# Performance work log

Hardware: AMD Instinct MI355X
Metric: run time of the kernel (lower is better)

The kernel has to match this reference:

```python
import jax, jax.numpy as jnp
import numpy as np

D_FEATURE = 512
D_K = 512
B, LQ, N = 64, 128, 2048
NEG_BIAS = 1e10


def setup_inputs() -> dict:
    key = jax.random.key(0)
    k1, k2, k3, k4, k5, k6 = jax.random.split(key, 6)
    # xavier_uniform bound for Linear(d_feature -> d_k), weight shape [d_k, d_feature]
    bound = float(np.sqrt(6.0 / (D_FEATURE + D_K)))
    metal_feature = jax.random.normal(k1, (B, LQ, D_FEATURE), dtype=jnp.float32)
    x = jax.random.normal(k2, (B, N, D_FEATURE), dtype=jnp.float32)
    mask = jax.random.randint(k3, (B, N), 0, 2, dtype=jnp.int32)
    W_q = jax.random.uniform(k4, (D_K, D_FEATURE), jnp.float32, -bound, bound)
    W_k = jax.random.uniform(k5, (D_K, D_FEATURE), jnp.float32, -bound, bound)
    W_v = jax.random.uniform(k6, (D_K, D_FEATURE), jnp.float32, -bound, bound)
    return {"metal_feature": metal_feature, "x": x, "mask": mask,
            "W_q": W_q, "W_k": W_k, "W_v": W_v}


def reference(metal_feature, x, mask, W_q, W_k, W_v):
    # Q: [B, Lq, d_k], K/V: [B, N, d_k]  (torch Linear: y = x @ W.T, no bias)
    Q = jnp.einsum('blf,kf->blk', metal_feature, W_q)
    K = jnp.einsum('bnf,kf->bnk', x, W_k)
    V = jnp.einsum('bnf,kf->bnk', x, W_v)
    scale = 1.0 / jnp.sqrt(jnp.float32(D_K))
    # scores: [B, Lq, N] with additive mask bias (mask broadcast over queries)
    scores = jnp.einsum('blk,bnk->bln', Q, K) * scale
    scores = scores - (1.0 - mask[:, None, :].astype(scores.dtype)) * NEG_BIAS
    attn = jax.nn.softmax(scores, axis=-1)
    out = jnp.einsum('bln,bnk->blk', attn, V)
    # relu; squeeze(1) is a no-op for Lq>1; dropout identity at eval
    return jax.nn.relu(out)
```

## Files before the change

### kernel.cpp

```cpp
#include <hip/hip_runtime.h>

typedef __attribute__((ext_vector_type(4))) float   f32x4;
typedef __attribute__((ext_vector_type(8))) __bf16  bf16x8;
typedef unsigned short u16;
typedef __attribute__((ext_vector_type(8))) unsigned short u16x8;
typedef __attribute__((ext_vector_type(4))) unsigned short u16x4;

__device__ __forceinline__ u16 f2bf(float f) {
  unsigned u = __builtin_bit_cast(unsigned, f);
  u += 0x7fffu + ((u >> 16) & 1u);
  return (u16)(u >> 16);
}
__device__ __forceinline__ float bf2f(u16 h) {
  unsigned u = ((unsigned)h) << 16;
  return __builtin_bit_cast(float, u);
}
__device__ __forceinline__ void gld16(const void* g, void* l) {
  __builtin_amdgcn_global_load_lds(
      (const __attribute__((address_space(1))) void*)g,
      (__attribute__((address_space(3))) void*)l, 16, 0, 0);
}


#define SB __builtin_amdgcn_sched_barrier(0)
#define SYNC_MID do { SB; __builtin_amdgcn_s_barrier(); \
  asm volatile("s_waitcnt lgkmcnt(0)" ::: "memory"); SB; } while(0)
#define SYNC_END do { SB; __builtin_amdgcn_s_barrier(); SB; } while(0)
#define VM4 do { SB; asm volatile("s_waitcnt vmcnt(4)" ::: "memory"); SB; } while(0)
#define VM0 do { SB; asm volatile("s_waitcnt vmcnt(0)" ::: "memory"); SB; } while(0)

#define LDA(AQ, S, I0) \
  _Pragma("unroll") for (int f = 0; f < 2; ++f) \
  _Pragma("unroll") for (int s = 0; s < 2; ++s) { \
    const int rl = ((I0)+f)*16 + lr; \
    AQ[f*2+s] = *(const u16x8*)&SM[((S)*2 + wr)*8192 + rl*64 + (((s*4+lc) ^ (rl&7))*8)]; }

#define LDB(S) \
  _Pragma("unroll") for (int j = 0; j < 4; ++j) \
  _Pragma("unroll") for (int s = 0; s < 2; ++s) { \
    const int rl = (wc&1)*64 + j*16 + lr; \
    bq[j][s] = *(const u16x8*)&SM[32768 + ((S)*2 + (wc>>1))*8192 + rl*64 + (((s*4+lc) ^ (rl&7))*8)]; }

#define MM(AQ, I0) do { \
  _Pragma("unroll") for (int f = 0; f < 2; ++f) \
  _Pragma("unroll") for (int j = 0; j < 4; ++j) \
  _Pragma("unroll") for (int s = 0; s < 2; ++s) \
    acc[(I0)+f][j] = __builtin_amdgcn_mfma_f32_16x16x32_bf16( \
      __builtin_bit_cast(bf16x8, AQ[f*2+s]), __builtin_bit_cast(bf16x8, bq[j][s]), \
      acc[(I0)+f][j], 0, 0, 0); \
  } while(0)

__global__ __launch_bounds__(512, 1)
void kv8_k(const u16* __restrict__ xb, const u16* __restrict__ Wkv,
           u16* __restrict__ Kc, u16* __restrict__ Vt)
{
  __shared__ u16 SM[65536];
  const int t = threadIdx.x;
  const int w = t >> 6, lane = t & 63;
  const int wr = w >> 2, wc = w & 3;
  const int lr = lane & 15, lc = lane >> 4;

  int bx, by;
  if (gridDim.y == 64) {
    const int h = (int)(blockIdx.y * 4 + blockIdx.x);
    const int c = h & 7, i = h >> 3;
    by = c + 8 * (i & 7);
    bx = i >> 3;
  } else { bx = blockIdx.x; by = blockIdx.y; }
  const int n0 = bx * 256;
  const u16* xg = xb + (long)by * 2048 * 512;

  f32x4 acc[8][4];
#pragma unroll
  for (int i = 0; i < 8; i++)
#pragma unroll
    for (int j = 0; j < 4; j++) acc[i][j] = f32x4{0.f, 0.f, 0.f, 0.f};
  u16x8 bq[4][2];

  auto stageA = [&](int TT, int h) {
#pragma unroll
    for (int r = 0; r < 2; ++r) {
      const int c = r * 512 + t;
      const int row = c >> 3, slot = c & 7;
      const u16* g = xg + (long)((TT >> 3) * 256 + h * 128 + row) * 512
                        + (TT & 7) * 64 + ((slot ^ (row & 7)) * 8);
      gld16(g, (void*)&SM[((TT & 1) * 2 + h) * 8192 + c * 8]);
    }
  };
  auto stageB = [&](int TT, int h) {
#pragma unroll
    for (int r = 0; r < 2; ++r) {
      const int c = r * 512 + t;
      const int row = c >> 3, slot = c & 7;
      const u16* g = Wkv + (long)(n0 + h * 128 + row) * 512
                         + (TT & 7) * 64 + ((slot ^ (row & 7)) * 8);
      gld16(g, (void*)&SM[32768 + ((TT & 1) * 2 + h) * 8192 + c * 8]);
    }
  };
  auto epi = [&](int mt) {
#pragma unroll
    for (int i = 0; i < 8; i++)
#pragma unroll
      for (int j = 0; j < 4; j++) {
        const int ml = mt * 256 + wr * 128 + i * 16 + lc * 4;
        const int n  = n0 + wc * 64 + j * 16 + lr;
        if (n0 < 512) {
#pragma unroll
          for (int ii = 0; ii < 4; ii++)
            Kc[((long)by * 2048 + ml + ii) * 512 + n] = f2bf(acc[i][j][ii]);
        } else {
          u16x4 hh;
#pragma unroll
          for (int ii = 0; ii < 4; ii++) hh[ii] = f2bf(acc[i][j][ii]);
          *(u16x4*)(Vt + ((long)by * 512 + (n - 512)) * 2048 + ml) = hh;
        }
        acc[i][j] = f32x4{0.f, 0.f, 0.f, 0.f};
      }
  };

  stageA(0, 0); stageA(0, 1);
  stageB(0, 0); stageB(0, 1);
  stageB(1, 0); stageB(1, 1);
  VM4;
  __builtin_amdgcn_s_barrier(); SB;

  const int NT = 64;
#pragma unroll 1
  for (int I = 0; I < NT / 2; ++I) {
    const int a = 2 * I, b = 2 * I + 1;
    const bool g2 = (a + 2) < NT;
    const bool g3 = (b + 2) < NT;
    { u16x8 aqX[4], aqY[4];
      LDB(0); LDA(aqX, 0, 0); LDA(aqY, 0, 2);
      stageA(b, 0); stageA(b, 1);
      SYNC_MID;
      __builtin_amdgcn_s_setprio(1); MM(aqX, 0); MM(aqY, 2); __builtin_amdgcn_s_setprio(0);
      SYNC_END; }
    { u16x8 aqX[4], aqY[4];
      LDA(aqX, 0, 4); LDA(aqY, 0, 6);
      if (g2) { stageB(a + 2, 0); stageB(a + 2, 1); }
      SYNC_MID;
      __builtin_amdgcn_s_setprio(1); MM(aqX, 4); MM(aqY, 6); __builtin_amdgcn_s_setprio(0);
      if (g2) { VM4; } else { VM0; }
      SYNC_END; }
    { u16x8 aqX[4], aqY[4];
      LDB(1); LDA(aqX, 1, 0); LDA(aqY, 1, 2);
      if (g2) { stageA(a + 2, 0); stageA(a + 2, 1); }
      SYNC_MID;
      __builtin_amdgcn_s_setprio(1); MM(aqX, 0); MM(aqY, 2); __builtin_amdgcn_s_setprio(0);
      SYNC_END; }
    { u16x8 aqX[4], aqY[4];
      LDA(aqX, 1, 4); LDA(aqY, 1, 6);
      if (g3) { stageB(b + 2, 0); stageB(b + 2, 1); }
      SYNC_MID;
      __builtin_amdgcn_s_setprio(1); MM(aqX, 4); MM(aqY, 6); __builtin_amdgcn_s_setprio(0);
      if (g3) { VM4; } else { VM0; }
      SYNC_END; }
    if ((I & 3) == 3) epi(I >> 2);
  }
}

template<int EPI>
__global__ __launch_bounds__(256)
void gemm_k(const u16* __restrict__ Ap, const u16* __restrict__ Bp,
            void* __restrict__ Cp, const int* __restrict__ maskp,
            int K, long sA, long sB, long sC, long sM, int ldc, float scale)
{
  __shared__ u16 Asb[2][4096];
  __shared__ u16 Bs [2][4096];

  const int t = threadIdx.x, z = blockIdx.z;
  const int n0 = blockIdx.x * 128, m0 = blockIdx.y * 128;
  const int KT = K / 32;
  const u16* Ab = Ap + (long)z * sA;
  const u16* Bb = Bp + (long)z * sB;

  const int w = t >> 6, lane = t & 63;
  const int m0w = (w >> 1) * 64, n0w = (w & 1) * 64;
  const int lr = lane & 15, lc = lane >> 4;

  f32x4 acc[4][4];
#pragma unroll
  for (int i = 0; i < 4; i++)
#pragma unroll
    for (int j = 0; j < 4; j++) acc[i][j] = f32x4{0.f, 0.f, 0.f, 0.f};

  auto stage = [&](int buf, int kt) {
#pragma unroll
    for (int i = 0; i < 2; i++) {
      int chunk = w * 2 + i, row = chunk * 16 + (lane >> 2), cc = lane & 3;
      const u16* g = Ab + (long)(m0 + row) * K + kt * 32 + ((cc ^ ((row >> 1) & 3)) << 3);
      gld16(g, (void*)&Asb[buf][chunk * 512]);
    }
#pragma unroll
    for (int i = 0; i < 2; i++) {
      int chunk = w * 2 + i, row = chunk * 16 + (lane >> 2), cc = lane & 3;
      const u16* g = Bb + (long)(n0 + row) * K + kt * 32 + ((cc ^ ((row >> 1) & 3)) << 3);
      gld16(g, (void*)&Bs[buf][chunk * 512]);
    }
  };
  auto compute = [&](int buf) {
    bf16x8 af[4], bv[4];
#pragma unroll
    for (int f = 0; f < 4; f++) {
      const int R = m0w + f * 16 + lr;
      af[f] = __builtin_bit_cast(bf16x8,
          *(const u16x8*)&Asb[buf][R * 32 + ((lc ^ ((R >> 1) & 3)) << 3)]);
      const int R2 = n0w + f * 16 + lr;
      bv[f] = __builtin_bit_cast(bf16x8,
          *(const u16x8*)&Bs[buf][R2 * 32 + ((lc ^ ((R2 >> 1) & 3)) << 3)]);
    }
#pragma unroll
    for (int i = 0; i < 4; i++)
#pragma unroll
      for (int j = 0; j < 4; j++)
        acc[i][j] = __builtin_amdgcn_mfma_f32_16x16x32_bf16(af[i], bv[j], acc[i][j], 0, 0, 0);
  };

  stage(0, 0);
  __syncthreads();
  int cur = 0;
  for (int kt = 1; kt < KT; ++kt) {
    stage(cur ^ 1, kt);
    compute(cur);
    __syncthreads();
    cur ^= 1;
  }
  compute(cur);

#pragma unroll
  for (int i = 0; i < 4; i++) {
#pragma unroll
    for (int j = 0; j < 4; j++) {
      const int mb = m0 + m0w + i * 16 + lc * 4;
      const int n  = n0 + n0w + j * 16 + lr;
      if constexpr (EPI == 0) {
        u16* C = (u16*)Cp + (long)z * sC;
#pragma unroll
        for (int ii = 0; ii < 4; ii++)
          C[(long)(mb + ii) * ldc + n] = f2bf(acc[i][j][ii]);
      } else if constexpr (EPI == 2) {
        const int* mk = maskp + (long)z * sM;
        u16* C = (u16*)Cp + (long)z * sC;
        const float bias = mk[n] ? 0.f : -1e10f;
#pragma unroll
        for (int ii = 0; ii < 4; ii++)
          C[(long)(mb + ii) * ldc + n] = f2bf(acc[i][j][ii] * scale + bias);
      } else {
        float* C = (float*)Cp + (long)z * sC;
#pragma unroll
        for (int ii = 0; ii < 4; ii++)
          C[(long)(mb + ii) * ldc + n] = fmaxf(acc[i][j][ii], 0.f);
      }
    }
  }
}

__global__ __launch_bounds__(256)
void wconv_k(const float* __restrict__ Wq, const float* __restrict__ Wk,
             const float* __restrict__ Wv, u16* __restrict__ Wb)
{
  long i4 = (long)blockIdx.x * 256 + threadIdx.x;
  long e  = i4 * 4;
  const float* W = (e < 262144) ? Wq : (e < 524288 ? Wk : Wv);
  long off = e & 262143;
  f32x4 f = *(const f32x4*)(W + off);
  u16x4 h;
#pragma unroll
  for (int j = 0; j < 4; j++) h[j] = f2bf(f[j]);
  *(u16x4*)(Wb + e) = h;
}

__global__ __launch_bounds__(256)
void cvt_k(const float* __restrict__ in, u16* __restrict__ out)
{
  long i = ((long)blockIdx.x * 256 + threadIdx.x) * 8;
  f32x4 a = *(const f32x4*)(in + i);
  f32x4 b = *(const f32x4*)(in + i + 4);
  u16x8 h;
#pragma unroll
  for (int j = 0; j < 4; j++) { h[j] = f2bf(a[j]); h[4 + j] = f2bf(b[j]); }
  *(u16x8*)(out + i) = h;
}

__global__ __launch_bounds__(256)
void softmax_k(u16* __restrict__ S)
{
  const long row = blockIdx.x;
  const int  t   = threadIdx.x;
  u16* R = S + row * 2048;
  u16x8 v = *(const u16x8*)(R + t * 8);
  float f[8];
#pragma unroll
  for (int j = 0; j < 8; j++) f[j] = bf2f(v[j]);
  float m = f[0];
#pragma unroll
  for (int j = 1; j < 8; j++) m = fmaxf(m, f[j]);
#pragma unroll
  for (int off = 32; off > 0; off >>= 1) m = fmaxf(m, __shfl_xor(m, off));
  __shared__ float red[4], red2[4];
  const int w = t >> 6;
  if ((t & 63) == 0) red[w] = m;
  __syncthreads();
  m = fmaxf(fmaxf(red[0], red[1]), fmaxf(red[2], red[3]));
  float e[8], s = 0.f;
#pragma unroll
  for (int j = 0; j < 8; j++) { e[j] = __expf(f[j] - m); s += e[j]; }
#pragma unroll
  for (int off = 32; off > 0; off >>= 1) s += __shfl_xor(s, off);
  if ((t & 63) == 0) red2[w] = s;
  __syncthreads();
  s = red2[0] + red2[1] + red2[2] + red2[3];
  const float inv = 1.f / s;
  u16x8 o;
#pragma unroll
  for (int j = 0; j < 8; j++) o[j] = f2bf(e[j] * inv);
  *(u16x8*)(R + t * 8) = o;
}

extern "C" void kernel_launch(void* const* d_in, const int* in_sizes, int n_in,
                              void* d_out, int out_size, void* d_ws, size_t ws_size,
                              hipStream_t stream)
{
  const float* mf   = (const float*)d_in[0];
  const float* x    = (const float*)d_in[1];
  const int*   mask = (const int*)d_in[2];
  const float* Wq   = (const float*)d_in[3];
  const float* Wk   = (const float*)d_in[4];
  const float* Wv   = (const float*)d_in[5];
  float* out = (float*)d_out;

  u16* ws  = (u16*)d_ws;
  u16* Wb  = ws;
  u16* mfb = Wb + 786432;
  u16* Qb  = mfb + 4194304;
  u16* dyn = Qb + 4194304;

  const size_t fixedB = (size_t)(786432 + 4194304 + 4194304) * 2;
  int CB = 64;
  while (CB > 1 && fixedB + (size_t)CB * 6815744ull > ws_size) CB >>= 1;

  u16* xbc = dyn;
  u16* Kc  = xbc + (size_t)CB * 1048576;
  u16* Vtc = Kc  + (size_t)CB * 1048576;
  u16* Sc  = Vtc + (size_t)CB * 1048576;

  const float scale = 0.044194173824159216f;

  wconv_k<<<768, 256, 0, stream>>>(Wq, Wk, Wv, Wb);
  cvt_k<<<2048, 256, 0, stream>>>(mf, mfb);

  gemm_k<0><<<dim3(4, 64, 1), 256, 0, stream>>>(
      mfb, Wb, Qb, nullptr, 512, 0, 0, 0, 0, 512, 1.f);

  for (int bc = 0; bc < 64; bc += CB) {
    const float* xc = x + (long)bc * 2048 * 512;
    cvt_k<<<CB * 512, 256, 0, stream>>>(xc, xbc);
    kv8_k<<<dim3(4, CB, 1), 512, 0, stream>>>(xbc, Wb + 262144, Kc, Vtc);
    gemm_k<2><<<dim3(16, 1, CB), 256, 0, stream>>>(
        Qb + (long)bc * 65536, Kc, Sc, mask + (long)bc * 2048,
        512, 65536, 1048576, 262144, 2048, 2048, scale);
    softmax_k<<<CB * 128, 256, 0, stream>>>(Sc);
    gemm_k<3><<<dim3(4, 1, CB), 256, 0, stream>>>(
        Sc, Vtc, out + (long)bc * 65536, nullptr,
        2048, 262144, 1048576, 65536, 0, 512, 1.f);
  }
}
```

Baseline: 393.8 us.

## Fuse fp32-to-bf16 conversion of x into the K/V projection kernel

```diff
diff --git a/kernel.cpp b/kernel.cpp
--- a/kernel.cpp
+++ b/kernel.cpp
@@ -23,8 +23,8 @@
 
 
 #define SB __builtin_amdgcn_sched_barrier(0)
-#define SYNC_MID do { SB; __builtin_amdgcn_s_barrier(); \
-  asm volatile("s_waitcnt lgkmcnt(0)" ::: "memory"); SB; } while(0)
+#define LK0 asm volatile("s_waitcnt lgkmcnt(0)" ::: "memory")
+#define SYNC_MID do { SB; __builtin_amdgcn_s_barrier(); LK0; SB; } while(0)
 #define SYNC_END do { SB; __builtin_amdgcn_s_barrier(); SB; } while(0)
 #define VM4 do { SB; asm volatile("s_waitcnt vmcnt(4)" ::: "memory"); SB; } while(0)
 #define VM0 do { SB; asm volatile("s_waitcnt vmcnt(0)" ::: "memory"); SB; } while(0)
@@ -51,7 +51,7 @@
   } while(0)
 
 __global__ __launch_bounds__(512, 1)
-void kv8_k(const u16* __restrict__ xb, const u16* __restrict__ Wkv,
+void kv8_k(const float* __restrict__ x, const u16* __restrict__ Wkv,
            u16* __restrict__ Kc, u16* __restrict__ Vt)
 {
   __shared__ u16 SM[65536];
@@ -68,7 +68,7 @@
     bx = i >> 3;
   } else { bx = blockIdx.x; by = blockIdx.y; }
   const int n0 = bx * 256;
-  const u16* xg = xb + (long)by * 2048 * 512;
+  const float* xg = x + (long)by * 2048 * 512;
 
   f32x4 acc[8][4];
 #pragma unroll
@@ -77,14 +77,20 @@
     for (int j = 0; j < 4; j++) acc[i][j] = f32x4{0.f, 0.f, 0.f, 0.f};
   u16x8 bq[4][2];
 
-  auto stageA = [&](int TT, int h) {
-#pragma unroll
-    for (int r = 0; r < 2; ++r) {
-      const int c = r * 512 + t;
-      const int row = c >> 3, slot = c & 7;
-      const u16* g = xg + (long)((TT >> 3) * 256 + h * 128 + row) * 512
-                        + (TT & 7) * 64 + ((slot ^ (row & 7)) * 8);
-      gld16(g, (void*)&SM[((TT & 1) * 2 + h) * 8192 + c * 8]);
+  auto stageA = [&](int TT) {
+#pragma unroll
+    for (int r = 0; r < 4; ++r) {
+      const int p = r * 512 + t;
+      const int row = p >> 3, s = p & 7;
+      const float* g = xg + (long)((TT >> 3) * 256 + row) * 512
+                          + (TT & 7) * 64 + s * 8;
+      const f32x4 lo = *(const f32x4*)g;
+      const f32x4 hi = *(const f32x4*)(g + 4);
+      bf16x8 v;
+#pragma unroll
+      for (int j = 0; j < 4; ++j) { v[j] = (__bf16)lo[j]; v[4 + j] = (__bf16)hi[j]; }
+      *(u16x8*)&SM[((TT & 1) * 2 + (row >> 7)) * 8192 + (row & 127) * 64
+                   + ((s ^ (row & 7)) * 8)] = __builtin_bit_cast(u16x8, v);
     }
   };
   auto stageB = [&](int TT, int h) {
@@ -118,9 +124,10 @@
       }
   };
 
-  stageA(0, 0); stageA(0, 1);
+  stageA(0);
   stageB(0, 0); stageB(0, 1);
   stageB(1, 0); stageB(1, 1);
+  LK0; SB;
   VM4;
   __builtin_amdgcn_s_barrier(); SB;
 
@@ -132,7 +139,7 @@
     const bool g3 = (b + 2) < NT;
     { u16x8 aqX[4], aqY[4];
       LDB(0); LDA(aqX, 0, 0); LDA(aqY, 0, 2);
-      stageA(b, 0); stageA(b, 1);
+      stageA(b);
       SYNC_MID;
       __builtin_amdgcn_s_setprio(1); MM(aqX, 0); MM(aqY, 2); __builtin_amdgcn_s_setprio(0);
       SYNC_END; }
@@ -145,7 +152,7 @@
       SYNC_END; }
     { u16x8 aqX[4], aqY[4];
       LDB(1); LDA(aqX, 1, 0); LDA(aqY, 1, 2);
-      if (g2) { stageA(a + 2, 0); stageA(a + 2, 1); }
+      if (g2) stageA(a + 2);
       SYNC_MID;
       __builtin_amdgcn_s_setprio(1); MM(aqX, 0); MM(aqY, 2); __builtin_amdgcn_s_setprio(0);
       SYNC_END; }
@@ -338,11 +345,10 @@
 
   const size_t fixedB = (size_t)(786432 + 4194304 + 4194304) * 2;
   int CB = 64;
-  while (CB > 1 && fixedB + (size_t)CB * 6815744ull > ws_size) CB >>= 1;
-
-  u16* xbc = dyn;
-  u16* Kc  = xbc + (size_t)CB * 1048576;
-  u16* Vtc = Kc  + (size_t)CB * 1048576;
+  while (CB > 1 && fixedB + (size_t)CB * 4718592ull > ws_size) CB >>= 1;
+
+  u16* Kc  = dyn;
+  u16* Vtc = Kc + (size_t)CB * 1048576;
   u16* Sc  = Vtc + (size_t)CB * 1048576;
 
   const float scale = 0.044194173824159216f;
@@ -355,8 +361,7 @@
 
   for (int bc = 0; bc < 64; bc += CB) {
     const float* xc = x + (long)bc * 2048 * 512;
-    cvt_k<<<CB * 512, 256, 0, stream>>>(xc, xbc);
-    kv8_k<<<dim3(4, CB, 1), 512, 0, stream>>>(xbc, Wb + 262144, Kc, Vtc);
+    kv8_k<<<dim3(4, CB, 1), 512, 0, stream>>>(xc, Wb + 262144, Kc, Vtc);
     gemm_k<2><<<dim3(16, 1, CB), 256, 0, stream>>>(
         Qb + (long)bc * 65536, Kc, Sc, mask + (long)bc * 2048,
         512, 65536, 1048576, 262144, 2048, 2048, scale);
```

Measured after the change: 486.2 us. +23.5%, slower.
